# Optimization experiments

Hardware: AMD Instinct MI355X
Metric: run time of the kernel (lower is better)

## Reference

```python
import jax, jax.numpy as jnp
import numpy as np


def conv2d(x, w, b):
    # x: [B,C,H,W], w: [O,C,K,K] (VALID, stride 1)
    out = jax.lax.conv_general_dilated(
        x, w, window_strides=(1, 1), padding='VALID',
        dimension_numbers=('NCHW', 'OIHW', 'NCHW'))
    return out + b[None, :, None, None]


def deform_conv2d(x, offset, w, b):
    # torchvision DeformConv2d semantics, offset_groups=1, stride=1, padding=0.
    # x: [B,C,H,W]; offset: [B, 2*K*K, Ho, Wo] with (dy, dx) interleaved per tap.
    B, C, H, W = x.shape
    O, _, K, _ = w.shape
    KK = K * K
    Ho, Wo = H - K + 1, W - K + 1
    off = offset.reshape(B, KK, 2, Ho, Wo)
    ky = (jnp.arange(KK) // K).astype(x.dtype)
    kx = (jnp.arange(KK) % K).astype(x.dtype)
    # sampling positions p0 + p_k + dp  -> [B, KK, Ho, Wo]
    py = ky[None, :, None, None] + jnp.arange(Ho, dtype=x.dtype)[None, None, :, None] + off[:, :, 0]
    px = kx[None, :, None, None] + jnp.arange(Wo, dtype=x.dtype)[None, None, None, :] + off[:, :, 1]
    y0 = jnp.floor(py)
    x0 = jnp.floor(px)
    wy = py - y0  # fractional parts
    wx = px - x0
    y0i = y0.astype(jnp.int32)
    x0i = x0.astype(jnp.int32)

    def corner(yi, xi):
        valid = ((yi >= 0) & (yi < H) & (xi >= 0) & (xi < W)).astype(x.dtype)
        yc = jnp.clip(yi, 0, H - 1)
        xc = jnp.clip(xi, 0, W - 1)
        # per-batch gather over all channels -> [B, C, KK, Ho, Wo]
        g = jax.vmap(lambda im, a, bb: im[:, a, bb])(x, yc, xc)
        return g * valid[:, None]

    v00 = corner(y0i, x0i)
    v01 = corner(y0i, x0i + 1)
    v10 = corner(y0i + 1, x0i)
    v11 = corner(y0i + 1, x0i + 1)
    wy_ = wy[:, None]  # [B,1,KK,Ho,Wo]
    wx_ = wx[:, None]
    samp = (v00 * (1 - wy_) * (1 - wx_) + v01 * (1 - wy_) * wx_
            + v10 * wy_ * (1 - wx_) + v11 * wy_ * wx_)
    out = jnp.einsum('bckhw,ock->bohw', samp, w.reshape(O, C, KK))
    return out + b[None, :, None, None]


_STAGES = [
    # (in_ch, out_ch, K)
    (1, 16, 3), (16, 32, 3), (32, 16, 5), (16, 16, 7), (16, 8, 5), (8, 4, 3),
]


def setup_inputs() -> dict:
    key = jax.random.key(0)
    keys = iter(jax.random.split(key, 64))
    inp = {'x': jax.random.normal(next(keys), (512, 1, 33, 33), dtype=jnp.float32)}
    for i, (ci, co, k) in enumerate(_STAGES, start=1):
        # offset-predicting conv: small init so offsets stay near the regular grid
        inp[f'ow{i}'] = jax.random.normal(next(keys), (2 * k * k, ci, k, k), dtype=jnp.float32) * 0.05
        inp[f'ob{i}'] = jax.random.normal(next(keys), (2 * k * k,), dtype=jnp.float32) * 0.05
        scale = 1.0 / np.sqrt(ci * k * k)
        inp[f'w{i}'] = jax.random.normal(next(keys), (co, ci, k, k), dtype=jnp.float32) * scale
        inp[f'b{i}'] = jax.random.normal(next(keys), (co,), dtype=jnp.float32) * scale
    inp['fc1_w'] = jax.random.normal(next(keys), (256, 13 * 13 * 4), dtype=jnp.float32) * (1.0 / np.sqrt(676))
    inp['fc1_b'] = jnp.zeros((256,), dtype=jnp.float32)
    inp['fc2_w'] = jax.random.normal(next(keys), (10, 256), dtype=jnp.float32) * (1.0 / np.sqrt(256))
    inp['fc2_b'] = jnp.zeros((10,), dtype=jnp.float32)
    return inp


def reference(x, ow1, ob1, w1, b1, ow2, ob2, w2, b2, ow3, ob3, w3, b3,
              ow4, ob4, w4, b4, ow5, ob5, w5, b5, ow6, ob6, w6, b6,
              fc1_w, fc1_b, fc2_w, fc2_b):
    h = jax.nn.relu(deform_conv2d(x, conv2d(x, ow1, ob1), w1, b1))
    h = jax.nn.relu(deform_conv2d(h, conv2d(h, ow2, ob2), w2, b2))
    h = deform_conv2d(h, conv2d(h, ow3, ob3), w3, b3)  # NOTE: no ReLU on stage 3 (matches source)
    h = jax.nn.relu(deform_conv2d(h, conv2d(h, ow4, ob4), w4, b4))
    h = jax.nn.relu(deform_conv2d(h, conv2d(h, ow5, ob5), w5, b5))
    h = jax.nn.relu(deform_conv2d(h, conv2d(h, ow6, ob6), w6, b6))
    flat = h.reshape(h.shape[0], -1)  # [B, 4*13*13]
    z = jax.nn.relu(flat @ fc1_w.T + fc1_b)
    return z @ fc2_w.T + fc2_b
```

## Files before the change

kernel.cpp:

```cpp
#include <hip/hip_runtime.h>

typedef __attribute__((ext_vector_type(8))) short bf16x8;
typedef __attribute__((ext_vector_type(4))) float f32x4;
typedef unsigned short ushort_t;

__device__ inline ushort_t bf16_trunc(float f) { return (ushort_t)(__float_as_uint(f) >> 16); }
__device__ inline float bf16_to_f(ushort_t u) { return __uint_as_float(((unsigned int)u) << 16); }

template<int CI, int HW>
__global__ __launch_bounds__(256)
void convert_nhwc(const float* __restrict__ x, ushort_t* __restrict__ hi,
                  ushort_t* __restrict__ lo, int Mtotal)
{
    const int m = blockIdx.x * 256 + threadIdx.x;
    if (m >= Mtotal) return;
    const int b = m / HW, pos = m - b * HW;
    const float* xp = x + (size_t)b * CI * HW + pos;
    ushort_t* hp = hi + (size_t)m * CI;
    ushort_t* lp = lo + (size_t)m * CI;
#pragma unroll
    for (int ci = 0; ci < CI; ++ci) {
        const float v = xp[(size_t)ci * HW];
        const ushort_t h = bf16_trunc(v);
        hp[ci] = h;
        lp[ci] = bf16_trunc(v - bf16_to_f(h));
    }
}

template<int CI, int KK, int KKPAD, int NPAD, int OC>
__global__ __launch_bounds__(256)
void wprep(const float* __restrict__ w, ushort_t* __restrict__ bhi, ushort_t* __restrict__ blo)
{
    const int idx = blockIdx.x * 256 + threadIdx.x;
    if (idx >= KKPAD * NPAD * CI) return;
    const int kk  = idx / (NPAD * CI);
    const int rem = idx - kk * (NPAD * CI);
    const int n   = rem / CI;
    const int ci  = rem - n * CI;
    const float v = (kk < KK && n < OC) ? w[((size_t)n * CI + ci) * KK + kk] : 0.f;
    const ushort_t h = bf16_trunc(v);
    bhi[idx] = h;
    blo[idx] = bf16_trunc(v - bf16_to_f(h));
}

template<int CI, int KK, int TPAD, int NPAD, int OC>
__global__ __launch_bounds__(256)
void wprep_d(const float* __restrict__ w, ushort_t* __restrict__ bhi, ushort_t* __restrict__ blo)
{
    constexpr int NPASS = (CI + 7) / 8;
    constexpr int TOTAL = NPASS * TPAD * NPAD * 8;
    const int idx = blockIdx.x * 256 + threadIdx.x;
    if (idx >= TOTAL) return;
    const int j     = idx & 7;
    const int n     = (idx >> 3) % NPAD;
    const int kslot = (idx >> 3) / NPAD;
    const int pass  = kslot / TPAD;
    const int tap   = kslot - pass * TPAD;
    const int ci    = pass * 8 + j;
    const float v = (tap < KK && n < OC && ci < CI) ? w[((size_t)n * CI + ci) * KK + tap] : 0.f;
    const ushort_t h = bf16_trunc(v);
    bhi[idx] = h;
    blo[idx] = bf16_trunc(v - bf16_to_f(h));
}

template<int CI, int K, int H, int W, int Ho, int Wo, int OC, int NTTOT, int NT0, int KSTEPS>
__global__ __launch_bounds__(256)
void conv_mfma(const ushort_t* __restrict__ Xhi, const ushort_t* __restrict__ Xlo,
               const ushort_t* __restrict__ Bhi, const ushort_t* __restrict__ Blo,
               const float* __restrict__ bias, float* __restrict__ out, int Mtotal)
{
    constexpr int NPAD = NTTOT * 16;
    constexpr int HW   = H * W;
    constexpr int HoWo = Ho * Wo;
    constexpr int TKS  = 32 / CI;
    constexpr int ROWS = TKS * NT0 * 16;
    constexpr int BSTR = CI + 8;
    constexpr int CH8  = CI / 8;
    constexpr int CHUNKS = ROWS * CH8;

    __shared__ __align__(16) ushort_t sBh[2][ROWS * BSTR];
    __shared__ __align__(16) ushort_t sBl[2][ROWS * BSTR];

    const int tid  = threadIdx.x;
    const int lane = tid & 63;
    const int wid  = tid >> 6;
    const int col  = lane & 15;
    const int quad = lane >> 4;

    const int mBase  = blockIdx.x * 256 + wid * 64;
    const int ntBase = blockIdx.y * NT0;

    int aBase[4];
#pragma unroll
    for (int mt = 0; mt < 4; ++mt) {
        int mm = mBase + mt * 16 + col;
        if (mm >= Mtotal) mm = Mtotal - 1;
        const int b   = mm / HoWo;
        const int pos = mm - b * HoWo;
        const int oy  = pos / Wo;
        const int ox  = pos - oy * Wo;
        aBase[mt] = (b * HW + oy * W + ox) * CI;
    }

    f32x4 acc[4][NT0];
#pragma unroll
    for (int mt = 0; mt < 4; ++mt)
#pragma unroll
        for (int nt = 0; nt < NT0; ++nt) acc[mt][nt] = (f32x4){0.f, 0.f, 0.f, 0.f};

    auto loadSlab = [&](int ks, int buf) {
        const int tap0 = ks * TKS;
        for (int i = tid; i < CHUNKS; i += 256) {
            const int row = i / CH8;
            const int c8  = i - row * CH8;
            const int t   = row / (NT0 * 16);
            const int nn  = row - t * (NT0 * 16);
            int n = ntBase * 16 + nn;
            if (n > NPAD - 1) n = NPAD - 1;
            const int g = ((tap0 + t) * NPAD + n) * CI + c8 * 8;
            *(bf16x8*)(sBh[buf] + row * BSTR + c8 * 8) = *(const bf16x8*)(Bhi + g);
            *(bf16x8*)(sBl[buf] + row * BSTR + c8 * 8) = *(const bf16x8*)(Blo + g);
        }
    };

    loadSlab(0, 0);
    __syncthreads();

#pragma unroll
    for (int ks = 0; ks < KSTEPS; ++ks) {
        if (ks + 1 < KSTEPS) loadSlab(ks + 1, (ks + 1) & 1);

        const int k0   = ks * 32 + quad * 8;
        const int tap  = k0 / CI;
        const int tloc = tap - ks * TKS;
        const int ci   = k0 - tap * CI;
        const int dkk  = (tap / K) * W + (tap - (tap / K) * K);

        bf16x8 ah[4], al[4];
#pragma unroll
        for (int mt = 0; mt < 4; ++mt) {
            const int aoff = aBase[mt] + dkk * CI + ci;
            ah[mt] = *(const bf16x8*)(Xhi + aoff);
            al[mt] = *(const bf16x8*)(Xlo + aoff);
        }
        const ushort_t* __restrict__ bhp = sBh[ks & 1];
        const ushort_t* __restrict__ blp = sBl[ks & 1];
#pragma unroll
        for (int nt = 0; nt < NT0; ++nt) {
            const int ntg = ntBase + nt;
            if (ntg < NTTOT) {
                const int lrow = ((tloc * NT0 + nt) * 16 + col) * BSTR + ci;
                const bf16x8 bh = *(const bf16x8*)(bhp + lrow);
                const bf16x8 bl = *(const bf16x8*)(blp + lrow);
#pragma unroll
                for (int mt = 0; mt < 4; ++mt) {
                    acc[mt][nt] = __builtin_amdgcn_mfma_f32_16x16x32_bf16(ah[mt], bh, acc[mt][nt], 0, 0, 0);
                    acc[mt][nt] = __builtin_amdgcn_mfma_f32_16x16x32_bf16(al[mt], bh, acc[mt][nt], 0, 0, 0);
                    acc[mt][nt] = __builtin_amdgcn_mfma_f32_16x16x32_bf16(ah[mt], bl, acc[mt][nt], 0, 0, 0);
                }
            }
        }
        __syncthreads();
    }

#pragma unroll
    for (int mt = 0; mt < 4; ++mt) {
#pragma unroll
        for (int nt = 0; nt < NT0; ++nt) {
            const int ntg = ntBase + nt;
            const int n   = ntg * 16 + col;
            if (ntg < NTTOT && n < OC) {
                const float bv = bias[n];
#pragma unroll
                for (int r = 0; r < 4; ++r) {
                    const int m = mBase + mt * 16 + quad * 4 + r;
                    if (m < Mtotal) {
                        const int b   = m / HoWo;
                        const int pos = m - b * HoWo;
                        out[((size_t)b * OC + n) * HoWo + pos] = acc[mt][nt][r] + bv;
                    }
                }
            }
        }
    }
}

template<int K, int CI, int CO, int H, int W, int Ho, int Wo, bool RELU,
         int MT, int TPAD>
__global__ __launch_bounds__(MT * 64)
void deform_mfma(const float* __restrict__ x, const float* __restrict__ off,
                 const ushort_t* __restrict__ Bph, const ushort_t* __restrict__ Bpl,
                 const float* __restrict__ bias, float* __restrict__ out)
{
    constexpr int KK     = K * K;
    constexpr int HW     = H * W;
    constexpr int HoWo   = Ho * Wo;
    constexpr int NPASS  = CI / 8;
    constexpr int NT     = (CO + 15) / 16;
    constexpr int NPAD   = NT * 16;
    constexpr int STRIDE = 12;
    constexpr int nMB    = (HoWo + MT * 16 - 1) / (MT * 16);
    constexpr int THREADS = MT * 64;
    __shared__ __align__(16) float tile[HW * STRIDE];

    const int b    = blockIdx.x / nMB;
    const int mb   = blockIdx.x - b * nMB;
    const int tid  = threadIdx.x;
    const int wid  = tid >> 6;
    const int lane = tid & 63;
    const int col  = lane & 15;
    const int quad = lane >> 4;

    const int pixel0 = (mb * MT + wid) * 16;
    const int s      = pixel0 + col;
    const bool am    = (s < HoWo);
    const int oy = s / Wo, ox = s - oy * Wo;

    const float* offB = off + (size_t)b * 2 * KK * HoWo;

    f32x4 acc[NT];
#pragma unroll
    for (int nt = 0; nt < NT; ++nt) acc[nt] = (f32x4){0.f, 0.f, 0.f, 0.f};

    for (int pass = 0; pass < NPASS; ++pass) {
        const int cbase = pass * 8;
        __syncthreads();
        for (int pos = tid; pos < HW; pos += THREADS) {
#pragma unroll
            for (int c = 0; c < 8; ++c)
                tile[pos * STRIDE + c] = x[((size_t)b * CI + (cbase + c)) * HW + pos];
        }
        __syncthreads();

#pragma unroll
        for (int tg = 0; tg < TPAD / 4; ++tg) {
            const int tap = tg * 4 + quad;
            bf16x8 ahi = (bf16x8){0,0,0,0,0,0,0,0};
            bf16x8 alo = (bf16x8){0,0,0,0,0,0,0,0};

            if (am && tap < KK) {
                const float dy = offB[(size_t)(2 * tap + 0) * HoWo + s];
                const float dx = offB[(size_t)(2 * tap + 1) * HoWo + s];
                const float py = (float)(tap / K + oy) + dy;
                const float px = (float)(tap % K + ox) + dx;
                const float y0f = floorf(py), x0f = floorf(px);
                const float wy = py - y0f, wx = px - x0f;
                const int y0 = (int)y0f, x0 = (int)x0f;
                const int y1 = y0 + 1,   x1 = x0 + 1;

                const float m00 = (y0 >= 0 && y0 < H && x0 >= 0 && x0 < W) ? 1.f : 0.f;
                const float m01 = (y0 >= 0 && y0 < H && x1 >= 0 && x1 < W) ? 1.f : 0.f;
                const float m10 = (y1 >= 0 && y1 < H && x0 >= 0 && x0 < W) ? 1.f : 0.f;
                const float m11 = (y1 >= 0 && y1 < H && x1 >= 0 && x1 < W) ? 1.f : 0.f;

                const float w00 = (1.f - wy) * (1.f - wx) * m00;
                const float w01 = (1.f - wy) * wx         * m01;
                const float w10 = wy         * (1.f - wx) * m10;
                const float w11 = wy         * wx         * m11;

                const int y0c = min(max(y0, 0), H - 1), y1c = min(max(y1, 0), H - 1);
                const int x0c = min(max(x0, 0), W - 1), x1c = min(max(x1, 0), W - 1);
                const int i00 = (y0c * W + x0c) * STRIDE;
                const int i01 = (y0c * W + x1c) * STRIDE;
                const int i10 = (y1c * W + x0c) * STRIDE;
                const int i11 = (y1c * W + x1c) * STRIDE;

                float v00[8], v01[8], v10[8], v11[8];
                *(f32x4*)(v00) = *(const f32x4*)(tile + i00); *(f32x4*)(v00 + 4) = *(const f32x4*)(tile + i00 + 4);
                *(f32x4*)(v01) = *(const f32x4*)(tile + i01); *(f32x4*)(v01 + 4) = *(const f32x4*)(tile + i01 + 4);
                *(f32x4*)(v10) = *(const f32x4*)(tile + i10); *(f32x4*)(v10 + 4) = *(const f32x4*)(tile + i10 + 4);
                *(f32x4*)(v11) = *(const f32x4*)(tile + i11); *(f32x4*)(v11 + 4) = *(const f32x4*)(tile + i11 + 4);
#pragma unroll
                for (int j = 0; j < 8; ++j) {
                    const float sv = fmaf(v11[j], w11, fmaf(v10[j], w10,
                                     fmaf(v01[j], w01, v00[j] * w00)));
                    const ushort_t h = bf16_trunc(sv);
                    ahi[j] = (short)h;
                    alo[j] = (short)bf16_trunc(sv - bf16_to_f(h));
                }
            }

            const size_t kslot = (size_t)(pass * TPAD + tap);
#pragma unroll
            for (int nt = 0; nt < NT; ++nt) {
                const bf16x8 bh = *(const bf16x8*)(Bph + (kslot * NPAD + nt * 16 + col) * 8);
                const bf16x8 bl = *(const bf16x8*)(Bpl + (kslot * NPAD + nt * 16 + col) * 8);
                acc[nt] = __builtin_amdgcn_mfma_f32_16x16x32_bf16(ahi, bh, acc[nt], 0, 0, 0);
                acc[nt] = __builtin_amdgcn_mfma_f32_16x16x32_bf16(alo, bh, acc[nt], 0, 0, 0);
                acc[nt] = __builtin_amdgcn_mfma_f32_16x16x32_bf16(ahi, bl, acc[nt], 0, 0, 0);
            }
        }
    }

#pragma unroll
    for (int nt = 0; nt < NT; ++nt) {
        const int n = nt * 16 + col;
        if (n < CO) {
            const float bv = bias[n];
#pragma unroll
            for (int r = 0; r < 4; ++r) {
                const int m = pixel0 + quad * 4 + r;
                if (m < HoWo) {
                    float v = acc[nt][r] + bv;
                    if (RELU) v = fmaxf(v, 0.f);
                    out[((size_t)b * CO + n) * HoWo + m] = v;
                }
            }
        }
    }
}

template<int K, int CI, int CO, int H, int W, int Ho, int Wo, bool RELU,
         int CSPLIT, int STRIDE, int THREADS, int SPLIT>
__global__ __launch_bounds__(THREADS)
void deform_lds(const float* __restrict__ x, const float* __restrict__ off,
                const float* __restrict__ w, const float* __restrict__ bias,
                float* __restrict__ out)
{
    constexpr int KK    = K * K;
    constexpr int HW    = H * W;
    constexpr int HoWo  = Ho * Wo;
    constexpr int NPASS = CI / CSPLIT;
    constexpr int CHUNK = (HoWo + SPLIT - 1) / SPLIT;
    static_assert(CHUNK <= THREADS, "chunk must fit in one block");
    __shared__ __align__(16) float tile[HW * STRIDE];

    const int b   = blockIdx.x / SPLIT;
    const int sp  = blockIdx.x - b * SPLIT;
    const int tid = threadIdx.x;
    const int s   = sp * CHUNK + tid;
    const bool active = (tid < CHUNK) && (s < HoWo);

    const int oy = s / Wo, ox = s - oy * Wo;
    const float* offp = off + ((size_t)b * 2 * KK) * HoWo + s;

    float acc[CO];
#pragma unroll
    for (int o = 0; o < CO; ++o) acc[o] = 0.f;

    for (int pass = 0; pass < NPASS; ++pass) {
        const int cbase = pass * CSPLIT;
        __syncthreads();
        for (int pos = tid; pos < HW; pos += THREADS) {
#pragma unroll
            for (int c = 0; c < CSPLIT; ++c)
                tile[pos * STRIDE + c] = x[((size_t)b * CI + (cbase + c)) * HW + pos];
        }
        __syncthreads();

        if (active) {
            for (int kk = 0; kk < KK; ++kk) {
                const float dy = offp[(size_t)(2 * kk + 0) * HoWo];
                const float dx = offp[(size_t)(2 * kk + 1) * HoWo];
                const float py = (float)(kk / K + oy) + dy;
                const float px = (float)(kk % K + ox) + dx;
                const float y0f = floorf(py), x0f = floorf(px);
                const float wy = py - y0f, wx = px - x0f;
                const int y0 = (int)y0f, x0 = (int)x0f;
                const int y1 = y0 + 1,   x1 = x0 + 1;

                const float m00 = (y0 >= 0 && y0 < H && x0 >= 0 && x0 < W) ? 1.f : 0.f;
                const float m01 = (y0 >= 0 && y0 < H && x1 >= 0 && x1 < W) ? 1.f : 0.f;
                const float m10 = (y1 >= 0 && y1 < H && x0 >= 0 && x0 < W) ? 1.f : 0.f;
                const float m11 = (y1 >= 0 && y1 < H && x1 >= 0 && x1 < W) ? 1.f : 0.f;

                const float w00 = (1.f - wy) * (1.f - wx) * m00;
                const float w01 = (1.f - wy) * wx         * m01;
                const float w10 = wy         * (1.f - wx) * m10;
                const float w11 = wy         * wx         * m11;

                const int y0c = min(max(y0, 0), H - 1), y1c = min(max(y1, 0), H - 1);
                const int x0c = min(max(x0, 0), W - 1), x1c = min(max(x1, 0), W - 1);
                const int i00 = (y0c * W + x0c) * STRIDE;
                const int i01 = (y0c * W + x1c) * STRIDE;
                const int i10 = (y1c * W + x0c) * STRIDE;
                const int i11 = (y1c * W + x1c) * STRIDE;

                if constexpr (CSPLIT % 4 == 0) {
#pragma unroll
                    for (int cg = 0; cg < CSPLIT; cg += 4) {
                        const f32x4 v00 = *(const f32x4*)(tile + i00 + cg);
                        const f32x4 v01 = *(const f32x4*)(tile + i01 + cg);
                        const f32x4 v10 = *(const f32x4*)(tile + i10 + cg);
                        const f32x4 v11 = *(const f32x4*)(tile + i11 + cg);
#pragma unroll
                        for (int j = 0; j < 4; ++j) {
                            const float sv = fmaf(v11[j], w11, fmaf(v10[j], w10,
                                             fmaf(v01[j], w01, v00[j] * w00)));
#pragma unroll
                            for (int o = 0; o < CO; ++o)
                                acc[o] = fmaf(sv, w[(size_t)(o * CI + cbase + cg + j) * KK + kk], acc[o]);
                        }
                    }
                } else {
                    const float sv = fmaf(tile[i11], w11, fmaf(tile[i10], w10,
                                     fmaf(tile[i01], w01, tile[i00] * w00)));
#pragma unroll
                    for (int o = 0; o < CO; ++o)
                        acc[o] = fmaf(sv, w[(size_t)(o * CI + cbase) * KK + kk], acc[o]);
                }
            }
        }
    }

    if (active) {
        float* op = out + ((size_t)b * CO) * HoWo + s;
#pragma unroll
        for (int o = 0; o < CO; ++o) {
            float v = acc[o] + bias[o];
            if (RELU) v = fmaxf(v, 0.f);
            op[(size_t)o * HoWo] = v;
        }
    }
}

template<int K, int CI, int NOC, int OC, int H, int W, int Ho, int Wo, int PIX>
__global__ __launch_bounds__(256)
void conv_tile(const float* __restrict__ x, const float* __restrict__ w,
               const float* __restrict__ bias, float* __restrict__ out)
{
    constexpr int KK   = K * K;
    constexpr int HoWo = Ho * Wo;
    constexpr int WoG  = (Wo + PIX - 1) / PIX;
    constexpr int G    = Ho * WoG;
    constexpr int XV   = PIX + K - 1;

    const int oc0   = blockIdx.y * NOC;
    const int g_all = blockIdx.x * 256 + threadIdx.x;
    const int b     = g_all / G;
    const int g     = g_all - b * G;
    const int oy    = g / WoG;
    const int ox0   = (g - oy * WoG) * PIX;

    const float* xbp = x + (b * CI) * (H * W) + oy * W + ox0;
    const float* wp  = w + oc0 * (CI * KK);

    float acc[PIX][NOC];
#pragma unroll
    for (int p = 0; p < PIX; ++p)
#pragma unroll
        for (int j = 0; j < NOC; ++j) acc[p][j] = bias[oc0 + j];

    const int lim = W - 1 - ox0;

    for (int ci = 0; ci < CI; ++ci) {
        const float* xc = xbp + ci * (H * W);
#pragma unroll
        for (int ky = 0; ky < K; ++ky) {
            float xv[XV];
#pragma unroll
            for (int i = 0; i < XV; ++i) {
                const int off = (i <= lim) ? i : lim;
                xv[i] = xc[ky * W + off];
            }
#pragma unroll
            for (int kx = 0; kx < K; ++kx) {
#pragma unroll
                for (int p = 0; p < PIX; ++p) {
                    const float v = xv[p + kx];
#pragma unroll
                    for (int j = 0; j < NOC; ++j)
                        acc[p][j] = fmaf(v, wp[j * (CI * KK) + ci * KK + ky * K + kx], acc[p][j]);
                }
            }
        }
    }

    float* op = out + (b * OC + oc0) * HoWo + oy * Wo + ox0;
#pragma unroll
    for (int p = 0; p < PIX; ++p) {
        if (ox0 + p < Wo) {
#pragma unroll
            for (int j = 0; j < NOC; ++j) op[j * HoWo + p] = acc[p][j];
        }
    }
}

template<int IN, int OUT>
__global__ __launch_bounds__(256)
void wtrans(const float* __restrict__ w, float* __restrict__ wt)
{
    const int idx = blockIdx.x * 256 + threadIdx.x;
    if (idx >= IN * OUT) return;
    const int i = idx / OUT, j = idx - i * OUT;
    wt[idx] = w[(size_t)j * IN + i];
}

template<int IN, int OUT, bool RELU>
__global__ __launch_bounds__(256)
void fc_t(const float* __restrict__ h, const float* __restrict__ wt,
          const float* __restrict__ bias, float* __restrict__ out, int B)
{
    const int idx = blockIdx.x * 256 + threadIdx.x;
    if (idx >= B * OUT) return;
    const int b = idx / OUT;
    const int j = idx - b * OUT;
    const float* hb = h + (size_t)b * IN;
    float acc = bias[j];
#pragma unroll 4
    for (int i = 0; i < IN; ++i)
        acc = fmaf(hb[i], wt[(size_t)i * OUT + j], acc);
    if (RELU) acc = fmaxf(acc, 0.f);
    out[idx] = acc;
}

extern "C" void kernel_launch(void* const* d_in, const int* in_sizes, int n_in,
                              void* d_out, int out_size, void* d_ws, size_t ws_size,
                              hipStream_t stream)
{
    const int B = 512;
    const float* x = (const float*)d_in[0];
    const float *ow[6], *ob[6], *w[6], *bi[6];
    for (int i = 0; i < 6; ++i) {
        ow[i] = (const float*)d_in[1 + 4 * i];
        ob[i] = (const float*)d_in[2 + 4 * i];
        w[i]  = (const float*)d_in[3 + 4 * i];
        bi[i] = (const float*)d_in[4 + 4 * i];
    }
    const float* fc1w = (const float*)d_in[25];
    const float* fc1b = (const float*)d_in[26];
    const float* fc2w = (const float*)d_in[27];
    const float* fc2b = (const float*)d_in[28];
    float* out = (float*)d_out;

    float* P   = (float*)d_ws;
    float* Q   = P  + 14000000;
    float* OFF = Q  + 14000000;
    float* Z   = OFF + 18200000;
    ushort_t* WBhi = (ushort_t*)(Z + 200000);
    ushort_t* WBlo = WBhi + 200000;
    ushort_t* WDhi = WBlo + 200000;
    ushort_t* WDlo = WDhi + 200000;
    float* WT1 = (float*)(WDlo + 200000);
    float* WT2 = WT1 + 173056;

    const dim3 blk(256);
    #define GRIDT(Ho, Wo, PIX, NG) dim3((B * (Ho) * (((Wo) + (PIX) - 1) / (PIX)) + 255) / 256, (NG), 1)
    #define CEILDIV(a, b) (((a) + (b) - 1) / (b))

    conv_tile<3, 1, 6, 18, 33, 33, 31, 31, 4><<<GRIDT(31, 31, 4, 3), blk, 0, stream>>>(x, ow[0], ob[0], OFF);
    deform_lds<3, 1, 16, 33, 33, 31, 31, true, 1, 1, 512, 2><<<dim3(B * 2), dim3(512), 0, stream>>>(x, OFF, w[0], bi[0], P);

    {
        const int Mc = B * 961;
        const int Mv = B * 841;
        ushort_t* Xhi = (ushort_t*)Q;
        ushort_t* Xlo = Xhi + (size_t)(Mc + 2048) * 16;
        convert_nhwc<16, 961><<<CEILDIV(Mc, 256), blk, 0, stream>>>(P, Xhi, Xlo, Mc);
        wprep<16, 9, 10, 32, 18><<<CEILDIV(10 * 32 * 16, 256), blk, 0, stream>>>(ow[1], WBhi, WBlo);
        conv_mfma<16, 3, 31, 31, 29, 29, 18, 2, 2, 5><<<dim3(CEILDIV(Mv, 256), 1), blk, 0, stream>>>(Xhi, Xlo, WBhi, WBlo, ob[1], OFF, Mv);
        wprep_d<16, 9, 12, 32, 32><<<CEILDIV(2 * 12 * 32 * 8, 256), blk, 0, stream>>>(w[1], WDhi, WDlo);
        deform_mfma<3, 16, 32, 31, 31, 29, 29, true, 8, 12><<<dim3(B * 7), dim3(512), 0, stream>>>(P, OFF, WDhi, WDlo, bi[1], Q);
    }
    {
        const int Mc = B * 841;
        const int Mv = B * 625;
        ushort_t* Xhi = (ushort_t*)P;
        ushort_t* Xlo = Xhi + (size_t)(Mc + 2048) * 32;
        convert_nhwc<32, 841><<<CEILDIV(Mc, 256), blk, 0, stream>>>(Q, Xhi, Xlo, Mc);
        wprep<32, 25, 25, 64, 50><<<CEILDIV(25 * 64 * 32, 256), blk, 0, stream>>>(ow[2], WBhi, WBlo);
        conv_mfma<32, 5, 29, 29, 25, 25, 50, 4, 4, 25><<<dim3(CEILDIV(Mv, 256), 1), blk, 0, stream>>>(Xhi, Xlo, WBhi, WBlo, ob[2], OFF, Mv);
        wprep_d<32, 25, 28, 16, 16><<<CEILDIV(4 * 28 * 16 * 8, 256), blk, 0, stream>>>(w[2], WDhi, WDlo);
        deform_mfma<5, 32, 16, 29, 29, 25, 25, false, 8, 28><<<dim3(B * 5), dim3(512), 0, stream>>>(Q, OFF, WDhi, WDlo, bi[2], P);
    }
    {
        const int Mc = B * 625;
        const int Mv = B * 361;
        ushort_t* Xhi = (ushort_t*)Q;
        ushort_t* Xlo = Xhi + (size_t)(Mc + 2048) * 16;
        convert_nhwc<16, 625><<<CEILDIV(Mc, 256), blk, 0, stream>>>(P, Xhi, Xlo, Mc);
        wprep<16, 49, 50, 112, 98><<<CEILDIV(50 * 112 * 16, 256), blk, 0, stream>>>(ow[3], WBhi, WBlo);
        conv_mfma<16, 7, 25, 25, 19, 19, 98, 7, 4, 25><<<dim3(CEILDIV(Mv, 256), 2), blk, 0, stream>>>(Xhi, Xlo, WBhi, WBlo, ob[3], OFF, Mv);
        wprep_d<16, 49, 52, 16, 16><<<CEILDIV(2 * 52 * 16 * 8, 256), blk, 0, stream>>>(w[3], WDhi, WDlo);
        deform_mfma<7, 16, 16, 25, 25, 19, 19, true, 8, 52><<<dim3(B * 3), dim3(512), 0, stream>>>(P, OFF, WDhi, WDlo, bi[3], Q);
    }
    {
        const int Mc = B * 361;
        const int Mv = B * 225;
        ushort_t* Xhi = (ushort_t*)P;
        ushort_t* Xlo = Xhi + (size_t)(Mc + 2048) * 16;
        convert_nhwc<16, 361><<<CEILDIV(Mc, 256), blk, 0, stream>>>(Q, Xhi, Xlo, Mc);
        wprep<16, 25, 26, 64, 50><<<CEILDIV(26 * 64 * 16, 256), blk, 0, stream>>>(ow[4], WBhi, WBlo);
        conv_mfma<16, 5, 19, 19, 15, 15, 50, 4, 4, 13><<<dim3(CEILDIV(Mv, 256), 1), blk, 0, stream>>>(Xhi, Xlo, WBhi, WBlo, ob[4], OFF, Mv);
        wprep_d<16, 25, 28, 16, 8><<<CEILDIV(2 * 28 * 16 * 8, 256), blk, 0, stream>>>(w[4], WDhi, WDlo);
        deform_mfma<5, 16, 8, 19, 19, 15, 15, true, 4, 28><<<dim3(B * 4), dim3(256), 0, stream>>>(Q, OFF, WDhi, WDlo, bi[4], P);
    }
    conv_tile<3, 8, 6, 18, 15, 15, 13, 13, 4><<<GRIDT(13, 13, 4, 3), blk, 0, stream>>>(P, ow[5], ob[5], OFF);
    deform_lds<3, 8, 4, 15, 15, 13, 13, true, 8, 12, 192, 1><<<dim3(B), dim3(192), 0, stream>>>(P, OFF, w[5], bi[5], Q);

    wtrans<676, 256><<<CEILDIV(676 * 256, 256), blk, 0, stream>>>(fc1w, WT1);
    wtrans<256, 10><<<CEILDIV(256 * 10, 256), blk, 0, stream>>>(fc2w, WT2);
    fc_t<676, 256, true><<<dim3(CEILDIV(B * 256, 256)), blk, 0, stream>>>(Q, WT1, fc1b, Z, B);
    fc_t<256, 10, false><<<dim3(CEILDIV(B * 10, 256)), blk, 0, stream>>>(Z, WT2, fc2b, out, B);

    #undef GRIDT
    #undef CEILDIV
}
```

Measured before the change: 976.3 us.

## Fuse NHWC hi/lo bf16 split into deform conv epilogues, drop convert kernels

```diff
diff --git a/kernel.cpp b/kernel.cpp
--- a/kernel.cpp
+++ b/kernel.cpp
@@ -6,26 +6,6 @@
 
 __device__ inline ushort_t bf16_trunc(float f) { return (ushort_t)(__float_as_uint(f) >> 16); }
 __device__ inline float bf16_to_f(ushort_t u) { return __uint_as_float(((unsigned int)u) << 16); }
-
-template<int CI, int HW>
-__global__ __launch_bounds__(256)
-void convert_nhwc(const float* __restrict__ x, ushort_t* __restrict__ hi,
-                  ushort_t* __restrict__ lo, int Mtotal)
-{
-    const int m = blockIdx.x * 256 + threadIdx.x;
-    if (m >= Mtotal) return;
-    const int b = m / HW, pos = m - b * HW;
-    const float* xp = x + (size_t)b * CI * HW + pos;
-    ushort_t* hp = hi + (size_t)m * CI;
-    ushort_t* lp = lo + (size_t)m * CI;
-#pragma unroll
-    for (int ci = 0; ci < CI; ++ci) {
-        const float v = xp[(size_t)ci * HW];
-        const ushort_t h = bf16_trunc(v);
-        hp[ci] = h;
-        lp[ci] = bf16_trunc(v - bf16_to_f(h));
-    }
-}
 
 template<int CI, int KK, int KKPAD, int NPAD, int OC>
 __global__ __launch_bounds__(256)
@@ -186,11 +166,13 @@
 }
 
 template<int K, int CI, int CO, int H, int W, int Ho, int Wo, bool RELU,
-         int MT, int TPAD>
+         int MT, int TPAD, bool OUTPL>
 __global__ __launch_bounds__(MT * 64)
-void deform_mfma(const float* __restrict__ x, const float* __restrict__ off,
+void deform_mfma(const ushort_t* __restrict__ Xhi, const ushort_t* __restrict__ Xlo,
+                 const float* __restrict__ off,
                  const ushort_t* __restrict__ Bph, const ushort_t* __restrict__ Bpl,
-                 const float* __restrict__ bias, float* __restrict__ out)
+                 const float* __restrict__ bias,
+                 float* __restrict__ outF, ushort_t* __restrict__ oHi, ushort_t* __restrict__ oLo)
 {
     constexpr int KK     = K * K;
     constexpr int HW     = H * W;
@@ -226,9 +208,12 @@
         const int cbase = pass * 8;
         __syncthreads();
         for (int pos = tid; pos < HW; pos += THREADS) {
+            const size_t g = ((size_t)b * HW + pos) * CI + cbase;
+            const bf16x8 h8 = *(const bf16x8*)(Xhi + g);
+            const bf16x8 l8 = *(const bf16x8*)(Xlo + g);
 #pragma unroll
             for (int c = 0; c < 8; ++c)
-                tile[pos * STRIDE + c] = x[((size_t)b * CI + (cbase + c)) * HW + pos];
+                tile[pos * STRIDE + c] = bf16_to_f((ushort_t)h8[c]) + bf16_to_f((ushort_t)l8[c]);
         }
         __syncthreads();
 
@@ -303,7 +288,14 @@
                 if (m < HoWo) {
                     float v = acc[nt][r] + bv;
                     if (RELU) v = fmaxf(v, 0.f);
-                    out[((size_t)b * CO + n) * HoWo + m] = v;
+                    if (OUTPL) {
+                        const size_t o = ((size_t)b * HoWo + m) * CO + n;
+                        const ushort_t h = bf16_trunc(v);
+                        oHi[o] = h;
+                        oLo[o] = bf16_trunc(v - bf16_to_f(h));
+                    } else {
+                        outF[((size_t)b * CO + n) * HoWo + m] = v;
+                    }
                 }
             }
         }
@@ -311,11 +303,11 @@
 }
 
 template<int K, int CI, int CO, int H, int W, int Ho, int Wo, bool RELU,
-         int CSPLIT, int STRIDE, int THREADS, int SPLIT>
+         int CSPLIT, int STRIDE, int THREADS, int SPLIT, bool OUTPL>
 __global__ __launch_bounds__(THREADS)
 void deform_lds(const float* __restrict__ x, const float* __restrict__ off,
                 const float* __restrict__ w, const float* __restrict__ bias,
-                float* __restrict__ out)
+                float* __restrict__ outF, ushort_t* __restrict__ oHi, ushort_t* __restrict__ oLo)
 {
     constexpr int KK    = K * K;
     constexpr int HW    = H * W;
@@ -404,12 +396,18 @@
     }
 
     if (active) {
-        float* op = out + ((size_t)b * CO) * HoWo + s;
 #pragma unroll
         for (int o = 0; o < CO; ++o) {
             float v = acc[o] + bias[o];
             if (RELU) v = fmaxf(v, 0.f);
-            op[(size_t)o * HoWo] = v;
+            if (OUTPL) {
+                const size_t oi = ((size_t)b * HoWo + s) * CO + o;
+                const ushort_t h = bf16_trunc(v);
+                oHi[oi] = h;
+                oLo[oi] = bf16_trunc(v - bf16_to_f(h));
+            } else {
+                outF[((size_t)b * CO + o) * HoWo + s] = v;
+            }
         }
     }
 }
@@ -538,59 +536,48 @@
     #define GRIDT(Ho, Wo, PIX, NG) dim3((B * (Ho) * (((Wo) + (PIX) - 1) / (PIX)) + 255) / 256, (NG), 1)
     #define CEILDIV(a, b) (((a) + (b) - 1) / (b))
 
+    ushort_t* PL2h = (ushort_t*)Q;  ushort_t* PL2l = PL2h + (size_t)(B * 961 + 2048) * 16;
+    ushort_t* PL3h = (ushort_t*)P;  ushort_t* PL3l = PL3h + (size_t)(B * 841 + 2048) * 32;
+    ushort_t* PL4h = (ushort_t*)Q;  ushort_t* PL4l = PL4h + (size_t)(B * 625 + 2048) * 16;
+    ushort_t* PL5h = (ushort_t*)P;  ushort_t* PL5l = PL5h + (size_t)(B * 361 + 2048) * 16;
+
     conv_tile<3, 1, 6, 18, 33, 33, 31, 31, 4><<<GRIDT(31, 31, 4, 3), blk, 0, stream>>>(x, ow[0], ob[0], OFF);
-    deform_lds<3, 1, 16, 33, 33, 31, 31, true, 1, 1, 512, 2><<<dim3(B * 2), dim3(512), 0, stream>>>(x, OFF, w[0], bi[0], P);
+    deform_lds<3, 1, 16, 33, 33, 31, 31, true, 1, 1, 512, 2, true><<<dim3(B * 2), dim3(512), 0, stream>>>(x, OFF, w[0], bi[0], nullptr, PL2h, PL2l);
 
     {
-        const int Mc = B * 961;
         const int Mv = B * 841;
-        ushort_t* Xhi = (ushort_t*)Q;
-        ushort_t* Xlo = Xhi + (size_t)(Mc + 2048) * 16;
-        convert_nhwc<16, 961><<<CEILDIV(Mc, 256), blk, 0, stream>>>(P, Xhi, Xlo, Mc);
         wprep<16, 9, 10, 32, 18><<<CEILDIV(10 * 32 * 16, 256), blk, 0, stream>>>(ow[1], WBhi, WBlo);
-        conv_mfma<16, 3, 31, 31, 29, 29, 18, 2, 2, 5><<<dim3(CEILDIV(Mv, 256), 1), blk, 0, stream>>>(Xhi, Xlo, WBhi, WBlo, ob[1], OFF, Mv);
+        conv_mfma<16, 3, 31, 31, 29, 29, 18, 2, 2, 5><<<dim3(CEILDIV(Mv, 256), 1), blk, 0, stream>>>(PL2h, PL2l, WBhi, WBlo, ob[1], OFF, Mv);
         wprep_d<16, 9, 12, 32, 32><<<CEILDIV(2 * 12 * 32 * 8, 256), blk, 0, stream>>>(w[1], WDhi, WDlo);
-        deform_mfma<3, 16, 32, 31, 31, 29, 29, true, 8, 12><<<dim3(B * 7), dim3(512), 0, stream>>>(P, OFF, WDhi, WDlo, bi[1], Q);
+        deform_mfma<3, 16, 32, 31, 31, 29, 29, true, 8, 12, true><<<dim3(B * 7), dim3(512), 0, stream>>>(PL2h, PL2l, OFF, WDhi, WDlo, bi[1], nullptr, PL3h, PL3l);
     }
     {
-        const int Mc = B * 841;
         const int Mv = B * 625;
-        ushort_t* Xhi = (ushort_t*)P;
-        ushort_t* Xlo = Xhi + (size_t)(Mc + 2048) * 32;
-        convert_nhwc<32, 841><<<CEILDIV(Mc, 256), blk, 0, stream>>>(Q, Xhi, Xlo, Mc);
         wprep<32, 25, 25, 64, 50><<<CEILDIV(25 * 64 * 32, 256), blk, 0, stream>>>(ow[2], WBhi, WBlo);
-        conv_mfma<32, 5, 29, 29, 25, 25, 50, 4, 4, 25><<<dim3(CEILDIV(Mv, 256), 1), blk, 0, stream>>>(Xhi, Xlo, WBhi, WBlo, ob[2], OFF, Mv);
+        conv_mfma<32, 5, 29, 29, 25, 25, 50, 4, 4, 25><<<dim3(CEILDIV(Mv, 256), 1), blk, 0, stream>>>(PL3h, PL3l, WBhi, WBlo, ob[2], OFF, Mv);
         wprep_d<32, 25, 28, 16, 16><<<CEILDIV(4 * 28 * 16 * 8, 256), blk, 0, stream>>>(w[2], WDhi, WDlo);
-        deform_mfma<5, 32, 16, 29, 29, 25, 25, false, 8, 28><<<dim3(B * 5), dim3(512), 0, stream>>>(Q, OFF, WDhi, WDlo, bi[2], P);
+        deform_mfma<5, 32, 16, 29, 29, 25, 25, false, 8, 28, true><<<dim3(B * 5), dim3(512), 0, stream>>>(PL3h, PL3l, OFF, WDhi, WDlo, bi[2], nullptr, PL4h, PL4l);
     }
     {
-        const int Mc = B * 625;
         const int Mv = B * 361;
-        ushort_t* Xhi = (ushort_t*)Q;
-        ushort_t* Xlo = Xhi + (size_t)(Mc + 2048) * 16;
-        convert_nhwc<16, 625><<<CEILDIV(Mc, 256), blk, 0, stream>>>(P, Xhi, Xlo, Mc);
         wprep<16, 49, 50, 112, 98><<<CEILDIV(50 * 112 * 16, 256), blk, 0, stream>>>(ow[3], WBhi, WBlo);
-        conv_mfma<16, 7, 25, 25, 19, 19, 98, 7, 4, 25><<<dim3(CEILDIV(Mv, 256), 2), blk, 0, stream>>>(Xhi, Xlo, WBhi, WBlo, ob[3], OFF, Mv);
+        conv_mfma<16, 7, 25, 25, 19, 19, 98, 7, 4, 25><<<dim3(CEILDIV(Mv, 256), 2), blk, 0, stream>>>(PL4h, PL4l, WBhi, WBlo, ob[3], OFF, Mv);
         wprep_d<16, 49, 52, 16, 16><<<CEILDIV(2 * 52 * 16 * 8, 256), blk, 0, stream>>>(w[3], WDhi, WDlo);
-        deform_mfma<7, 16, 16, 25, 25, 19, 19, true, 8, 52><<<dim3(B * 3), dim3(512), 0, stream>>>(P, OFF, WDhi, WDlo, bi[3], Q);
+        deform_mfma<7, 16, 16, 25, 25, 19, 19, true, 8, 52, true><<<dim3(B * 3), dim3(512), 0, stream>>>(PL4h, PL4l, OFF, WDhi, WDlo, bi[3], nullptr, PL5h, PL5l);
     }
     {
-        const int Mc = B * 361;
         const int Mv = B * 225;
-        ushort_t* Xhi = (ushort_t*)P;
-        ushort_t* Xlo = Xhi + (size_t)(Mc + 2048) * 16;
-        convert_nhwc<16, 361><<<CEILDIV(Mc, 256), blk, 0, stream>>>(Q, Xhi, Xlo, Mc);
         wprep<16, 25, 26, 64, 50><<<CEILDIV(26 * 64 * 16, 256), blk, 0, stream>>>(ow[4], WBhi, WBlo);
-        conv_mfma<16, 5, 19, 19, 15, 15, 50, 4, 4, 13><<<dim3(CEILDIV(Mv, 256), 1), blk, 0, stream>>>(Xhi, Xlo, WBhi, WBlo, ob[4], OFF, Mv);
+        conv_mfma<16, 5, 19, 19, 15, 15, 50, 4, 4, 13><<<dim3(CEILDIV(Mv, 256), 1), blk, 0, stream>>>(PL5h, PL5l, WBhi, WBlo, ob[4], OFF, Mv);
         wprep_d<16, 25, 28, 16, 8><<<CEILDIV(2 * 28 * 16 * 8, 256), blk, 0, stream>>>(w[4], WDhi, WDlo);
-        deform_mfma<5, 16, 8, 19, 19, 15, 15, true, 4, 28><<<dim3(B * 4), dim3(256), 0, stream>>>(Q, OFF, WDhi, WDlo, bi[4], P);
-    }
-    conv_tile<3, 8, 6, 18, 15, 15, 13, 13, 4><<<GRIDT(13, 13, 4, 3), blk, 0, stream>>>(P, ow[5], ob[5], OFF);
-    deform_lds<3, 8, 4, 15, 15, 13, 13, true, 8, 12, 192, 1><<<dim3(B), dim3(192), 0, stream>>>(P, OFF, w[5], bi[5], Q);
+        deform_mfma<5, 16, 8, 19, 19, 15, 15, true, 4, 28, false><<<dim3(B * 4), dim3(256), 0, stream>>>(PL5h, PL5l, OFF, WDhi, WDlo, bi[4], Q, nullptr, nullptr);
+    }
+    conv_tile<3, 8, 6, 18, 15, 15, 13, 13, 4><<<GRIDT(13, 13, 4, 3), blk, 0, stream>>>(Q, ow[5], ob[5], OFF);
+    deform_lds<3, 8, 4, 15, 15, 13, 13, true, 8, 12, 192, 1, false><<<dim3(B), dim3(192), 0, stream>>>(Q, OFF, w[5], bi[5], P, nullptr, nullptr);
 
     wtrans<676, 256><<<CEILDIV(676 * 256, 256), blk, 0, stream>>>(fc1w, WT1);
     wtrans<256, 10><<<CEILDIV(256 * 10, 256), blk, 0, stream>>>(fc2w, WT2);
-    fc_t<676, 256, true><<<dim3(CEILDIV(B * 256, 256)), blk, 0, stream>>>(Q, WT1, fc1b, Z, B);
+    fc_t<676, 256, true><<<dim3(CEILDIV(B * 256, 256)), blk, 0, stream>>>(P, WT1, fc1b, Z, B);
     fc_t<256, 10, false><<<dim3(CEILDIV(B * 10, 256)), blk, 0, stream>>>(Z, WT2, fc2b, out, B);
 
     #undef GRIDT
```

New measurement: 1.005 ms. 1.03x slower.
